# Kernel optimization log

Hardware: AMD Instinct MI355X
Metric: run time of the kernel (lower is better)

Reference implementation:

```python
import jax, jax.numpy as jnp
import numpy as np

D_MODEL = 512
D_STATE = 32
EXPAND = 2
D_INNER = D_MODEL * EXPAND
BATCH = 2
SEQ_LEN = 1024


def setup_inputs() -> dict:
    key = jax.random.key(0)
    ks = jax.random.split(key, 8)
    s = lambda fan_in: 1.0 / np.sqrt(fan_in)
    x = jax.random.normal(ks[0], (BATCH, SEQ_LEN, D_MODEL), dtype=jnp.float32)
    Wx = jax.random.uniform(ks[1], (D_INNER, D_MODEL), minval=-s(D_MODEL), maxval=s(D_MODEL))
    Wdt = jax.random.uniform(ks[2], (D_INNER, D_MODEL), minval=-s(D_MODEL), maxval=s(D_MODEL))
    bdt = jax.random.uniform(ks[3], (D_INNER,)) + 1.0  # dt_proj.bias init: rand + 1
    A_log = jnp.log(jax.random.uniform(ks[4], (D_INNER, D_STATE), minval=1e-4, maxval=1.0))
    WB = jax.random.uniform(ks[5], (D_INNER * D_STATE, D_MODEL), minval=-s(D_MODEL), maxval=s(D_MODEL))
    WC = jax.random.uniform(ks[6], (D_INNER * D_STATE, D_MODEL), minval=-s(D_MODEL), maxval=s(D_MODEL))
    Wout = jax.random.uniform(ks[7], (D_MODEL, D_INNER), minval=-s(D_INNER), maxval=s(D_INNER))
    return {"x": x, "Wx": Wx, "Wdt": Wdt, "bdt": bdt, "A_log": A_log,
            "WB": WB, "WC": WC, "Wout": Wout}


def reference(x, Wx, Wdt, bdt, A_log, WB, WC, Wout):
    b, L, _ = x.shape
    d_inner, d_state = A_log.shape

    x_inner = jnp.einsum('bld,ed->ble', x, Wx)                 # (b, L, d_inner)
    delta = jax.nn.softplus(jnp.einsum('bld,ed->ble', x, Wdt) + bdt)
    A = -jnp.exp(A_log.astype(jnp.float32))                    # (d_inner, d_state)
    A_disc = jnp.exp(delta[..., None] * A)                     # (b, L, d_inner, d_state)
    Bm = jnp.einsum('bld,ed->ble', x, WB).reshape(b, L, d_inner, d_state)
    Cm = jnp.einsum('bld,ed->ble', x, WC).reshape(b, L, d_inner, d_state)

    def step(h, inp):
        a_t, b_t, c_t, x_t = inp
        h = a_t * h + b_t * x_t[..., None]                     # (b, d_inner, d_state)
        y = jnp.sum(c_t * h, axis=-1)                          # (b, d_inner)
        return h, y

    h0 = jnp.zeros((b, d_inner, d_state), dtype=x.dtype)
    xs = (jnp.moveaxis(A_disc, 1, 0), jnp.moveaxis(Bm, 1, 0),
          jnp.moveaxis(Cm, 1, 0), jnp.moveaxis(x_inner, 1, 0))
    _, ys = jax.lax.scan(step, h0, xs)                         # ys: (L, b, d_inner)
    y = jnp.moveaxis(ys, 0, 1)
    y = y * jax.nn.sigmoid(y)                                  # SiLU
    return jnp.einsum('ble,de->bld', y, Wout)
```

## Files before the change

### kernel.cpp

```cpp
#include <hip/hip_runtime.h>

#define BATCH   2
#define SEQLEN  1024
#define DMODEL  512
#define DSTATE  32
#define DINNER  1024
#define MROWS   (BATCH*SEQLEN)
#define NPROJ   (2*DINNER + 2*DINNER*DSTATE)

typedef short bf16x8 __attribute__((ext_vector_type(8)));
typedef float f32x4  __attribute__((ext_vector_type(4)));

__device__ __forceinline__ unsigned short f2bf(float f) {
    union { float f; unsigned u; } c; c.f = f;
    unsigned u = c.u;
    u += 0x7fffu + ((u >> 16) & 1u);
    return (unsigned short)(u >> 16);
}
__device__ __forceinline__ float bf2f(unsigned short h) {
    union { unsigned u; float f; } c; c.u = ((unsigned)h) << 16;
    return c.f;
}

__global__ void cast_all(const float4* __restrict__ Wx, const float4* __restrict__ Wdt,
                         const float4* __restrict__ WB, const float4* __restrict__ WC,
                         const float4* __restrict__ x,  const float4* __restrict__ Wout,
                         unsigned short* __restrict__ Wbf,
                         unsigned short* __restrict__ Xbf,
                         unsigned short* __restrict__ Woutbf) {
    const long nWx = 131072, nWdt = 131072, nWB = 4194304, nWC = 4194304;
    const long nWall = nWx + nWdt + nWB + nWC;
    const long nX = 262144, nWo = 131072;
    const long total = nWall + nX + nWo;
    for (long u = (long)blockIdx.x * blockDim.x + threadIdx.x; u < total;
         u += (long)gridDim.x * blockDim.x) {
        float4 v; unsigned short* dst;
        if (u < nWall) {
            if (u < nWx)             v = Wx[u];
            else if (u < nWx+nWdt)   v = Wdt[u - nWx];
            else if (u < nWx+nWdt+nWB) v = WB[u - nWx - nWdt];
            else                     v = WC[u - nWx - nWdt - nWB];
            dst = Wbf + u*4;
        } else if (u < nWall + nX) {
            v = x[u - nWall];       dst = Xbf + (u - nWall)*4;
        } else {
            v = Wout[u - nWall - nX]; dst = Woutbf + (u - nWall - nX)*4;
        }
        ushort4 o; o.x = f2bf(v.x); o.y = f2bf(v.y); o.z = f2bf(v.z); o.w = f2bf(v.w);
        *(ushort4*)dst = o;
    }
}

template<int EPI>
__global__ __launch_bounds__(256)
void gemm_bt(const unsigned short* __restrict__ A, const unsigned short* __restrict__ Bw,
             int K, int N, int t0, int Tchunk,
             float* __restrict__ xin, float* __restrict__ dlt,
             unsigned short* __restrict__ Bout, unsigned short* __restrict__ Cout,
             const float* __restrict__ bdt, float* __restrict__ outf) {
    __shared__ unsigned short Asm[2][128*32];
    __shared__ unsigned short Bsm[2][128*32];
    const int tid  = threadIdx.x;
    const int w    = tid >> 6;
    const int lane = tid & 63;
    const int wm   = w >> 1, wn = w & 1;

    const int nx = gridDim.x, ny = gridDim.y;
    int ntile, rtile;
    if ((nx & 7) == 0) {
        const int lin = blockIdx.x + nx * blockIdx.y;
        const int xcd = lin & 7;
        const int sl  = lin >> 3;
        ntile = xcd * (nx >> 3) + sl / ny;
        rtile = sl % ny;
    } else {
        ntile = blockIdx.x; rtile = blockIdx.y;
    }

    const int rr0  = rtile * 128;
    const int bb   = (rr0 >= Tchunk) ? 1 : 0;
    const int grow0 = bb * SEQLEN + t0 + (rr0 - bb * Tchunk);
    const int n0   = ntile * 128;

    f32x4 acc[4][4] = {};

    const unsigned short* Ag = A  + (size_t)grow0 * K;
    const unsigned short* Bg = Bw + (size_t)n0 * K;

    const int c0 = w*64 + lane;
    const int c1 = c0 + 256;
    const int r   = lane & 15;
    const int h16 = lane >> 4;

    const int rowc0 = c0 >> 2, rowc1 = c1 >> 2;
    const int subc0 = (c0 & 3) ^ ((c0 >> 3) & 3);
    const int subc1 = (c1 & 3) ^ ((c1 >> 3) & 3);
    const size_t srcA0 = (size_t)rowc0 * K + subc0 * 8;
    const size_t srcA1 = (size_t)rowc1 * K + subc1 * 8;

    const int nt = K >> 5;

    #define STAGE(k0_, buf_)                                                              \
        do {                                                                              \
            __builtin_amdgcn_global_load_lds(                                             \
                (const __attribute__((address_space(1))) void*)(Ag + srcA0 + (k0_)),      \
                (__attribute__((address_space(3))) void*)(&Asm[(buf_)][w*512]), 16, 0, 0);\
            __builtin_amdgcn_global_load_lds(                                             \
                (const __attribute__((address_space(1))) void*)(Ag + srcA1 + (k0_)),      \
                (__attribute__((address_space(3))) void*)(&Asm[(buf_)][2048 + w*512]), 16, 0, 0); \
            __builtin_amdgcn_global_load_lds(                                             \
                (const __attribute__((address_space(1))) void*)(Bg + srcA0 + (k0_)),      \
                (__attribute__((address_space(3))) void*)(&Bsm[(buf_)][w*512]), 16, 0, 0);\
            __builtin_amdgcn_global_load_lds(                                             \
                (const __attribute__((address_space(1))) void*)(Bg + srcA1 + (k0_)),      \
                (__attribute__((address_space(3))) void*)(&Bsm[(buf_)][2048 + w*512]), 16, 0, 0); \
        } while (0)

    #define COMPUTE(buf_)                                                                 \
        do {                                                                              \
            bf16x8 af[4], bfr[4];                                                         \
            _Pragma("unroll")                                                             \
            for (int i = 0; i < 4; i++) {                                                 \
                const int Ra = wm*64 + i*16 + r;                                          \
                const int Rb = wn*64 + i*16 + r;                                          \
                af[i]  = *(const bf16x8*)(&Asm[(buf_)][Ra*32 + (h16 ^ ((Ra>>1)&3))*8]);   \
                bfr[i] = *(const bf16x8*)(&Bsm[(buf_)][Rb*32 + (h16 ^ ((Rb>>1)&3))*8]);   \
            }                                                                             \
            _Pragma("unroll")                                                             \
            for (int i = 0; i < 4; i++)                                                   \
                _Pragma("unroll")                                                         \
                for (int j = 0; j < 4; j++)                                               \
                    acc[i][j] = __builtin_amdgcn_mfma_f32_16x16x32_bf16(af[i], bfr[j], acc[i][j], 0, 0, 0); \
        } while (0)

    STAGE(0, 0);
    for (int it = 0; it < nt - 1; ++it) {
        const int cur = it & 1;
        STAGE((it + 1) * 32, cur ^ 1);
        asm volatile("s_waitcnt vmcnt(4)" ::: "memory");
        __builtin_amdgcn_s_barrier();
        COMPUTE(cur);
        asm volatile("" ::: "memory");
        __builtin_amdgcn_s_barrier();
        asm volatile("" ::: "memory");
    }
    asm volatile("s_waitcnt vmcnt(0)" ::: "memory");
    __builtin_amdgcn_s_barrier();
    COMPUTE((nt - 1) & 1);

    #undef STAGE
    #undef COMPUTE

    const int q = lane >> 4;
    #pragma unroll
    for (int i = 0; i < 4; i++) {
        const int lr0 = wm*64 + i*16 + q*4;
        #pragma unroll
        for (int j = 0; j < 4; j++) {
            const int ncol = n0 + wn*64 + j*16 + r;
            if (EPI == 0) {
                const int cr   = rr0 + lr0;
                const int lt   = cr - bb*Tchunk;
                const size_t tb = (size_t)(lt >> 3);
                const int tin  = lt & 7;
                if (ncol < 1024) {
                    float4 o = {acc[i][j][0], acc[i][j][1], acc[i][j][2], acc[i][j][3]};
                    *(float4*)(xin + ((size_t)bb*(SEQLEN/8) + (t0>>3) + tb)*8192 + ncol*8 + tin) = o;
                } else if (ncol < 2048) {
                    const float bias = bdt[ncol - 1024];
                    float4 o;
                    {   float z0 = acc[i][j][0] + bias; o.x = (z0 > 20.f) ? z0 : log1pf(__expf(z0));
                        float z1 = acc[i][j][1] + bias; o.y = (z1 > 20.f) ? z1 : log1pf(__expf(z1));
                        float z2 = acc[i][j][2] + bias; o.z = (z2 > 20.f) ? z2 : log1pf(__expf(z2));
                        float z3 = acc[i][j][3] + bias; o.w = (z3 > 20.f) ? z3 : log1pf(__expf(z3)); }
                    *(float4*)(dlt + ((size_t)bb*(SEQLEN/8) + (t0>>3) + tb)*8192 + (ncol-1024)*8 + tin) = o;
                } else if (ncol < 34816) {
                    const int cb = ncol - 2048;
                    short4 o;
                    o.x = (short)f2bf(acc[i][j][0]); o.y = (short)f2bf(acc[i][j][1]);
                    o.z = (short)f2bf(acc[i][j][2]); o.w = (short)f2bf(acc[i][j][3]);
                    *(short4*)(Bout + ((size_t)bb*(Tchunk>>3) + tb)*262144 + (size_t)cb*8 + tin) = o;
                } else {
                    const int cc = ncol - 34816;
                    short4 o;
                    o.x = (short)f2bf(acc[i][j][0]); o.y = (short)f2bf(acc[i][j][1]);
                    o.z = (short)f2bf(acc[i][j][2]); o.w = (short)f2bf(acc[i][j][3]);
                    *(short4*)(Cout + ((size_t)bb*(Tchunk>>3) + tb)*262144 + (size_t)cc*8 + tin) = o;
                }
            } else {
                #pragma unroll
                for (int t = 0; t < 4; t++)
                    outf[(size_t)(grow0 + lr0 + t)*N + ncol] = acc[i][j][t];
            }
        }
    }
}

__global__ __launch_bounds__(256)
void scan_seg1(const float* __restrict__ dlt, const float* __restrict__ xin,
               const unsigned short* __restrict__ Bbf,
               const float* __restrict__ A_log,
               float* __restrict__ sc_h, float* __restrict__ sc_a,
               int t0, int Tchunk, int SEG, int Tg) {
    const int tid = threadIdx.x;
    const int g = tid >> 5, s = tid & 31;
    const int G = blockIdx.x * 8 + g;
    const int seg = blockIdx.y;
    const int b = G >> 10, e = G & 1023;

    const float Aes = -__expf(A_log[e*32 + s]);
    float h = 0.f, ap = 1.f;

    const int NT  = Tg >> 3;
    const int gt0 = (t0 + seg*Tg) >> 3;
    const int ct0 = (seg*Tg) >> 3;
    const float* dxp = dlt + ((size_t)b*(SEQLEN/8) + gt0)*8192 + e*8;
    const float* xxp = xin + ((size_t)b*(SEQLEN/8) + gt0)*8192 + e*8;
    const unsigned short* bp = Bbf + ((size_t)b*(Tchunk>>3) + ct0)*262144 + (size_t)(e*32+s)*8;

    float4 d0 = *(const float4*)dxp, d1 = *(const float4*)(dxp+4);
    float4 x0 = *(const float4*)xxp, x1 = *(const float4*)(xxp+4);
    bf16x8 bv = *(const bf16x8*)bp;

    for (int k = 0; k < NT; ++k) {
        float4 nd0, nd1, nx0, nx1; bf16x8 nbv;
        if (k + 1 < NT) {
            const float* p1 = dxp + (size_t)(k+1)*8192;
            nd0 = *(const float4*)p1; nd1 = *(const float4*)(p1+4);
            const float* p2 = xxp + (size_t)(k+1)*8192;
            nx0 = *(const float4*)p2; nx1 = *(const float4*)(p2+4);
            nbv = *(const bf16x8*)(bp + (size_t)(k+1)*262144);
        }
        const float db[8] = {d0.x,d0.y,d0.z,d0.w,d1.x,d1.y,d1.z,d1.w};
        const float xb[8] = {x0.x,x0.y,x0.z,x0.w,x1.x,x1.y,x1.z,x1.w};
        #pragma unroll
        for (int j = 0; j < 8; j++) {
            const float a = __expf(db[j] * Aes);
            h = a*h + bf2f((unsigned short)bv[j])*xb[j];
            ap *= a;
        }
        if (k + 1 < NT) { d0=nd0; d1=nd1; x0=nx0; x1=nx1; bv=nbv; }
    }
    sc_h[((size_t)G*SEG + seg)*32 + s] = h;
    sc_a[((size_t)G*SEG + seg)*32 + s] = ap;
}

__global__ __launch_bounds__(256)
void scan_seg2(const float* __restrict__ sc_h, const float* __restrict__ sc_a,
               float* __restrict__ sc_hin, float* __restrict__ hbuf,
               int SEG, int first) {
    const int idx = blockIdx.x * 256 + threadIdx.x;
    float h = first ? 0.f : hbuf[idx];
    const int G = idx >> 5, s = idx & 31;
    for (int seg = 0; seg < SEG; seg++) {
        const size_t o = ((size_t)G*SEG + seg)*32 + s;
        sc_hin[o] = h;
        h = sc_h[o] + sc_a[o]*h;
    }
    hbuf[idx] = h;
}

__global__ __launch_bounds__(256)
void scan_seg3(const float* __restrict__ dlt, const float* __restrict__ xin,
               const unsigned short* __restrict__ Bbf, const unsigned short* __restrict__ Cbf,
               const float* __restrict__ A_log, const float* __restrict__ sc_hin,
               unsigned short* __restrict__ Ybf,
               int t0, int Tchunk, int SEG, int Tg) {
    const int tid = threadIdx.x;
    const int g = tid >> 5, s = tid & 31;
    const int G = blockIdx.x * 8 + g;
    const int seg = blockIdx.y;
    const int b = G >> 10, e = G & 1023;

    const float Aes = -__expf(A_log[e*32 + s]);
    float h = sc_hin[((size_t)G*SEG + seg)*32 + s];

    const int NT  = Tg >> 3;
    const int gt0 = (t0 + seg*Tg) >> 3;
    const int ct0 = (seg*Tg) >> 3;
    const float* dxp = dlt + ((size_t)b*(SEQLEN/8) + gt0)*8192 + e*8;
    const float* xxp = xin + ((size_t)b*(SEQLEN/8) + gt0)*8192 + e*8;
    const unsigned short* bp = Bbf + ((size_t)b*(Tchunk>>3) + ct0)*262144 + (size_t)(e*32+s)*8;
    const unsigned short* cp = Cbf + ((size_t)b*(Tchunk>>3) + ct0)*262144 + (size_t)(e*32+s)*8;
    const int tbase = t0 + seg*Tg;

    float4 d0 = *(const float4*)dxp, d1 = *(const float4*)(dxp+4);
    float4 x0 = *(const float4*)xxp, x1 = *(const float4*)(xxp+4);
    bf16x8 bv = *(const bf16x8*)bp, cv = *(const bf16x8*)cp;

    for (int k = 0; k < NT; ++k) {
        float4 nd0, nd1, nx0, nx1; bf16x8 nbv, ncv;
        if (k + 1 < NT) {
            const float* p1 = dxp + (size_t)(k+1)*8192;
            nd0 = *(const float4*)p1; nd1 = *(const float4*)(p1+4);
            const float* p2 = xxp + (size_t)(k+1)*8192;
            nx0 = *(const float4*)p2; nx1 = *(const float4*)(p2+4);
            nbv = *(const bf16x8*)(bp + (size_t)(k+1)*262144);
            ncv = *(const bf16x8*)(cp + (size_t)(k+1)*262144);
        }
        const float db[8] = {d0.x,d0.y,d0.z,d0.w,d1.x,d1.y,d1.z,d1.w};
        const float xb[8] = {x0.x,x0.y,x0.z,x0.w,x1.x,x1.y,x1.z,x1.w};
        float p[8];
        #pragma unroll
        for (int j = 0; j < 8; j++) {
            const float a = __expf(db[j] * Aes);
            h = a*h + bf2f((unsigned short)bv[j])*xb[j];
            p[j] = bf2f((unsigned short)cv[j])*h;
        }
        #pragma unroll
        for (int i = 0; i < 4; i++) {
            float send = (s & 16) ? p[i] : p[i+4];
            float recv = __shfl_xor(send, 16, 32);
            p[i] = ((s & 16) ? p[i+4] : p[i]) + recv;
        }
        #pragma unroll
        for (int i = 0; i < 2; i++) {
            float send = (s & 8) ? p[i] : p[i+2];
            float recv = __shfl_xor(send, 8, 32);
            p[i] = ((s & 8) ? p[i+2] : p[i]) + recv;
        }
        {
            float send = (s & 4) ? p[0] : p[1];
            float recv = __shfl_xor(send, 4, 32);
            p[0] = ((s & 4) ? p[1] : p[0]) + recv;
        }
        p[0] += __shfl_xor(p[0], 2, 32);
        p[0] += __shfl_xor(p[0], 1, 32);
        if ((s & 3) == 0) {
            const int tl = s >> 2;
            const float qv = p[0];
            const float y = qv * __builtin_amdgcn_rcpf(1.f + __expf(-qv));
            Ybf[(size_t)b*1048576 + e + (size_t)(tbase + k*8 + tl)*1024] = f2bf(y);
        }
        if (k + 1 < NT) { d0=nd0; d1=nd1; x0=nx0; x1=nx1; bv=nbv; cv=ncv; }
    }
}

extern "C" void kernel_launch(void* const* d_in, const int* in_sizes, int n_in,
                              void* d_out, int out_size, void* d_ws, size_t ws_size,
                              hipStream_t stream) {
    const float* x     = (const float*)d_in[0];
    const float* Wx    = (const float*)d_in[1];
    const float* Wdt   = (const float*)d_in[2];
    const float* bdt   = (const float*)d_in[3];
    const float* A_log = (const float*)d_in[4];
    const float* WB    = (const float*)d_in[5];
    const float* WC    = (const float*)d_in[6];
    const float* Wout  = (const float*)d_in[7];

    char* ws = (char*)d_ws;
    unsigned short* Wbf    = (unsigned short*)(ws);
    unsigned short* Xbf    = (unsigned short*)(ws + 69206016);
    unsigned short* Woutbf = (unsigned short*)(ws + 71303168);
    float*          xin    = (float*)        (ws + 72351744);
    float*          dlt    = (float*)        (ws + 80740352);
    unsigned short* Ybf    = (unsigned short*)(ws + 89128960);
    float*          hbuf   = (float*)        (ws + 93323264);
    float*          sc_h   = (float*)        (ws + 93585408);
    float*          sc_a   = (float*)        (ws + 95682560);
    float*          sc_hin = (float*)        (ws + 97779712);
    unsigned short* Bbf    = (unsigned short*)(ws + 99876864);
    const size_t fixedB = 99876864;

    int T = 128;
    const int cands[4] = {1024, 512, 256, 128};
    for (int ci = 0; ci < 4; ci++) {
        if (fixedB + (size_t)2 * cands[ci] * 131072 <= ws_size) { T = cands[ci]; break; }
    }
    unsigned short* Cbf = Bbf + (size_t)T * 65536;

    const int SEG = 8;
    const int Tg = T / SEG;

    cast_all<<<dim3(2048), dim3(256), 0, stream>>>(
        (const float4*)Wx, (const float4*)Wdt, (const float4*)WB, (const float4*)WC,
        (const float4*)x, (const float4*)Wout, Wbf, Xbf, Woutbf);

    const int NC = SEQLEN / T;
    for (int c = 0; c < NC; c++) {
        const int t0 = c * T;
        gemm_bt<0><<<dim3(NPROJ/128, 2*T/128), dim3(256), 0, stream>>>(
            Xbf, Wbf, DMODEL, NPROJ, t0, T, xin, dlt, Bbf, Cbf, bdt, nullptr);
        scan_seg1<<<dim3(256, SEG), dim3(256), 0, stream>>>(
            dlt, xin, Bbf, A_log, sc_h, sc_a, t0, T, SEG, Tg);
        scan_seg2<<<dim3(256), dim3(256), 0, stream>>>(
            sc_h, sc_a, sc_hin, hbuf, SEG, (c == 0) ? 1 : 0);
        scan_seg3<<<dim3(256, SEG), dim3(256), 0, stream>>>(
            dlt, xin, Bbf, Cbf, A_log, sc_hin, Ybf, t0, T, SEG, Tg);
    }

    gemm_bt<1><<<dim3(DMODEL/128, MROWS/128), dim3(256), 0, stream>>>(
        Ybf, Woutbf, DINNER, DMODEL, 0, MROWS, nullptr, nullptr, nullptr, nullptr, nullptr,
        (float*)d_out);
}
```

Measured before the change: 409.3 us.

## Store scan inputs segment-contiguous so each channel's time series is sequential

The projection GEMM epilogue now writes xin, delta, B and C in a layout grouped by (batch, segment, channel), with each channel's timesteps for one segment stored contiguously. Previously consecutive 8-step blocks sat 8192 or 262144 elements apart. Each scan thread now walks a short contiguous stream, which should improve cache and page locality for the scan kernels. In exchange the GEMM epilogue writes are more scattered, since different segments map to distant addresses. xin and delta are now chunk-local buffers.

```diff
diff --git a/kernel.cpp b/kernel.cpp
--- a/kernel.cpp
+++ b/kernel.cpp
@@ -54,7 +54,7 @@
 template<int EPI>
 __global__ __launch_bounds__(256)
 void gemm_bt(const unsigned short* __restrict__ A, const unsigned short* __restrict__ Bw,
-             int K, int N, int t0, int Tchunk,
+             int K, int N, int t0, int Tchunk, int tgs,
              float* __restrict__ xin, float* __restrict__ dlt,
              unsigned short* __restrict__ Bout, unsigned short* __restrict__ Cout,
              const float* __restrict__ bdt, float* __restrict__ outf) {
@@ -152,6 +152,8 @@
     #undef COMPUTE
 
     const int q = lane >> 4;
+    const int Tg  = 1 << tgs;
+    const int NT  = Tg >> 3;
     #pragma unroll
     for (int i = 0; i < 4; i++) {
         const int lr0 = wm*64 + i*16 + q*4;
@@ -161,11 +163,14 @@
             if (EPI == 0) {
                 const int cr   = rr0 + lr0;
                 const int lt   = cr - bb*Tchunk;
-                const size_t tb = (size_t)(lt >> 3);
-                const int tin  = lt & 7;
+                const int seg  = lt >> tgs;
+                const int tloc = lt & (Tg - 1);
+                const int kin  = tloc >> 3;
+                const int tin  = tloc & 7;
+                const int bs   = bb*8 + seg;
                 if (ncol < 1024) {
                     float4 o = {acc[i][j][0], acc[i][j][1], acc[i][j][2], acc[i][j][3]};
-                    *(float4*)(xin + ((size_t)bb*(SEQLEN/8) + (t0>>3) + tb)*8192 + ncol*8 + tin) = o;
+                    *(float4*)(xin + ((size_t)bs*1024 + ncol)*Tg + tloc) = o;
                 } else if (ncol < 2048) {
                     const float bias = bdt[ncol - 1024];
                     float4 o;
@@ -173,19 +178,19 @@
                         float z1 = acc[i][j][1] + bias; o.y = (z1 > 20.f) ? z1 : log1pf(__expf(z1));
                         float z2 = acc[i][j][2] + bias; o.z = (z2 > 20.f) ? z2 : log1pf(__expf(z2));
                         float z3 = acc[i][j][3] + bias; o.w = (z3 > 20.f) ? z3 : log1pf(__expf(z3)); }
-                    *(float4*)(dlt + ((size_t)bb*(SEQLEN/8) + (t0>>3) + tb)*8192 + (ncol-1024)*8 + tin) = o;
+                    *(float4*)(dlt + ((size_t)bs*1024 + (ncol-1024))*Tg + tloc) = o;
                 } else if (ncol < 34816) {
-                    const int cb = ncol - 2048;
+                    const int es = ncol - 2048;
                     short4 o;
                     o.x = (short)f2bf(acc[i][j][0]); o.y = (short)f2bf(acc[i][j][1]);
                     o.z = (short)f2bf(acc[i][j][2]); o.w = (short)f2bf(acc[i][j][3]);
-                    *(short4*)(Bout + ((size_t)bb*(Tchunk>>3) + tb)*262144 + (size_t)cb*8 + tin) = o;
+                    *(short4*)(Bout + (((size_t)bs*1024 + (es>>5))*NT + kin)*256 + (es&31)*8 + tin) = o;
                 } else {
-                    const int cc = ncol - 34816;
+                    const int es = ncol - 34816;
                     short4 o;
                     o.x = (short)f2bf(acc[i][j][0]); o.y = (short)f2bf(acc[i][j][1]);
                     o.z = (short)f2bf(acc[i][j][2]); o.w = (short)f2bf(acc[i][j][3]);
-                    *(short4*)(Cout + ((size_t)bb*(Tchunk>>3) + tb)*262144 + (size_t)cc*8 + tin) = o;
+                    *(short4*)(Cout + (((size_t)bs*1024 + (es>>5))*NT + kin)*256 + (es&31)*8 + tin) = o;
                 }
             } else {
                 #pragma unroll
@@ -201,7 +206,7 @@
                const unsigned short* __restrict__ Bbf,
                const float* __restrict__ A_log,
                float* __restrict__ sc_h, float* __restrict__ sc_a,
-               int t0, int Tchunk, int SEG, int Tg) {
+               int Tg) {
     const int tid = threadIdx.x;
     const int g = tid >> 5, s = tid & 31;
     const int G = blockIdx.x * 8 + g;
@@ -211,25 +216,22 @@
     const float Aes = -__expf(A_log[e*32 + s]);
     float h = 0.f, ap = 1.f;
 
-    const int NT  = Tg >> 3;
-    const int gt0 = (t0 + seg*Tg) >> 3;
-    const int ct0 = (seg*Tg) >> 3;
-    const float* dxp = dlt + ((size_t)b*(SEQLEN/8) + gt0)*8192 + e*8;
-    const float* xxp = xin + ((size_t)b*(SEQLEN/8) + gt0)*8192 + e*8;
-    const unsigned short* bp = Bbf + ((size_t)b*(Tchunk>>3) + ct0)*262144 + (size_t)(e*32+s)*8;
-
-    float4 d0 = *(const float4*)dxp, d1 = *(const float4*)(dxp+4);
-    float4 x0 = *(const float4*)xxp, x1 = *(const float4*)(xxp+4);
+    const int NT = Tg >> 3;
+    const int bs = b*8 + seg;
+    const float* dp = dlt + ((size_t)bs*1024 + e)*Tg;
+    const float* xp = xin + ((size_t)bs*1024 + e)*Tg;
+    const unsigned short* bp = Bbf + ((size_t)bs*1024 + e)*NT*256 + s*8;
+
+    float4 d0 = *(const float4*)dp, d1 = *(const float4*)(dp+4);
+    float4 x0 = *(const float4*)xp, x1 = *(const float4*)(xp+4);
     bf16x8 bv = *(const bf16x8*)bp;
 
     for (int k = 0; k < NT; ++k) {
         float4 nd0, nd1, nx0, nx1; bf16x8 nbv;
         if (k + 1 < NT) {
-            const float* p1 = dxp + (size_t)(k+1)*8192;
-            nd0 = *(const float4*)p1; nd1 = *(const float4*)(p1+4);
-            const float* p2 = xxp + (size_t)(k+1)*8192;
-            nx0 = *(const float4*)p2; nx1 = *(const float4*)(p2+4);
-            nbv = *(const bf16x8*)(bp + (size_t)(k+1)*262144);
+            nd0 = *(const float4*)(dp + (k+1)*8); nd1 = *(const float4*)(dp + (k+1)*8 + 4);
+            nx0 = *(const float4*)(xp + (k+1)*8); nx1 = *(const float4*)(xp + (k+1)*8 + 4);
+            nbv = *(const bf16x8*)(bp + (size_t)(k+1)*256);
         }
         const float db[8] = {d0.x,d0.y,d0.z,d0.w,d1.x,d1.y,d1.z,d1.w};
         const float xb[8] = {x0.x,x0.y,x0.z,x0.w,x1.x,x1.y,x1.z,x1.w};
@@ -241,19 +243,19 @@
         }
         if (k + 1 < NT) { d0=nd0; d1=nd1; x0=nx0; x1=nx1; bv=nbv; }
     }
-    sc_h[((size_t)G*SEG + seg)*32 + s] = h;
-    sc_a[((size_t)G*SEG + seg)*32 + s] = ap;
+    sc_h[((size_t)G*8 + seg)*32 + s] = h;
+    sc_a[((size_t)G*8 + seg)*32 + s] = ap;
 }
 
 __global__ __launch_bounds__(256)
 void scan_seg2(const float* __restrict__ sc_h, const float* __restrict__ sc_a,
                float* __restrict__ sc_hin, float* __restrict__ hbuf,
-               int SEG, int first) {
+               int first) {
     const int idx = blockIdx.x * 256 + threadIdx.x;
     float h = first ? 0.f : hbuf[idx];
     const int G = idx >> 5, s = idx & 31;
-    for (int seg = 0; seg < SEG; seg++) {
-        const size_t o = ((size_t)G*SEG + seg)*32 + s;
+    for (int seg = 0; seg < 8; seg++) {
+        const size_t o = ((size_t)G*8 + seg)*32 + s;
         sc_hin[o] = h;
         h = sc_h[o] + sc_a[o]*h;
     }
@@ -265,7 +267,7 @@
                const unsigned short* __restrict__ Bbf, const unsigned short* __restrict__ Cbf,
                const float* __restrict__ A_log, const float* __restrict__ sc_hin,
                unsigned short* __restrict__ Ybf,
-               int t0, int Tchunk, int SEG, int Tg) {
+               int t0, int Tg) {
     const int tid = threadIdx.x;
     const int g = tid >> 5, s = tid & 31;
     const int G = blockIdx.x * 8 + g;
@@ -273,30 +275,27 @@
     const int b = G >> 10, e = G & 1023;
 
     const float Aes = -__expf(A_log[e*32 + s]);
-    float h = sc_hin[((size_t)G*SEG + seg)*32 + s];
-
-    const int NT  = Tg >> 3;
-    const int gt0 = (t0 + seg*Tg) >> 3;
-    const int ct0 = (seg*Tg) >> 3;
-    const float* dxp = dlt + ((size_t)b*(SEQLEN/8) + gt0)*8192 + e*8;
-    const float* xxp = xin + ((size_t)b*(SEQLEN/8) + gt0)*8192 + e*8;
-    const unsigned short* bp = Bbf + ((size_t)b*(Tchunk>>3) + ct0)*262144 + (size_t)(e*32+s)*8;
-    const unsigned short* cp = Cbf + ((size_t)b*(Tchunk>>3) + ct0)*262144 + (size_t)(e*32+s)*8;
+    float h = sc_hin[((size_t)G*8 + seg)*32 + s];
+
+    const int NT = Tg >> 3;
+    const int bs = b*8 + seg;
+    const float* dp = dlt + ((size_t)bs*1024 + e)*Tg;
+    const float* xp = xin + ((size_t)bs*1024 + e)*Tg;
+    const unsigned short* bp = Bbf + ((size_t)bs*1024 + e)*NT*256 + s*8;
+    const unsigned short* cp = Cbf + ((size_t)bs*1024 + e)*NT*256 + s*8;
     const int tbase = t0 + seg*Tg;
 
-    float4 d0 = *(const float4*)dxp, d1 = *(const float4*)(dxp+4);
-    float4 x0 = *(const float4*)xxp, x1 = *(const float4*)(xxp+4);
+    float4 d0 = *(const float4*)dp, d1 = *(const float4*)(dp+4);
+    float4 x0 = *(const float4*)xp, x1 = *(const float4*)(xp+4);
     bf16x8 bv = *(const bf16x8*)bp, cv = *(const bf16x8*)cp;
 
     for (int k = 0; k < NT; ++k) {
         float4 nd0, nd1, nx0, nx1; bf16x8 nbv, ncv;
         if (k + 1 < NT) {
-            const float* p1 = dxp + (size_t)(k+1)*8192;
-            nd0 = *(const float4*)p1; nd1 = *(const float4*)(p1+4);
-            const float* p2 = xxp + (size_t)(k+1)*8192;
-            nx0 = *(const float4*)p2; nx1 = *(const float4*)(p2+4);
-            nbv = *(const bf16x8*)(bp + (size_t)(k+1)*262144);
-            ncv = *(const bf16x8*)(cp + (size_t)(k+1)*262144);
+            nd0 = *(const float4*)(dp + (k+1)*8); nd1 = *(const float4*)(dp + (k+1)*8 + 4);
+            nx0 = *(const float4*)(xp + (k+1)*8); nx1 = *(const float4*)(xp + (k+1)*8 + 4);
+            nbv = *(const bf16x8*)(bp + (size_t)(k+1)*256);
+            ncv = *(const bf16x8*)(cp + (size_t)(k+1)*256);
         }
         const float db[8] = {d0.x,d0.y,d0.z,d0.w,d1.x,d1.y,d1.z,d1.w};
         const float xb[8] = {x0.x,x0.y,x0.z,x0.w,x1.x,x1.y,x1.z,x1.w};
@@ -369,8 +368,8 @@
     }
     unsigned short* Cbf = Bbf + (size_t)T * 65536;
 
-    const int SEG = 8;
-    const int Tg = T / SEG;
+    const int Tg = T / 8;
+    int tgs = 0; while ((1 << tgs) < Tg) tgs++;
 
     cast_all<<<dim3(2048), dim3(256), 0, stream>>>(
         (const float4*)Wx, (const float4*)Wdt, (const float4*)WB, (const float4*)WC,
@@ -380,16 +379,16 @@
     for (int c = 0; c < NC; c++) {
         const int t0 = c * T;
         gemm_bt<0><<<dim3(NPROJ/128, 2*T/128), dim3(256), 0, stream>>>(
-            Xbf, Wbf, DMODEL, NPROJ, t0, T, xin, dlt, Bbf, Cbf, bdt, nullptr);
-        scan_seg1<<<dim3(256, SEG), dim3(256), 0, stream>>>(
-            dlt, xin, Bbf, A_log, sc_h, sc_a, t0, T, SEG, Tg);
+            Xbf, Wbf, DMODEL, NPROJ, t0, T, tgs, xin, dlt, Bbf, Cbf, bdt, nullptr);
+        scan_seg1<<<dim3(256, 8), dim3(256), 0, stream>>>(
+            dlt, xin, Bbf, A_log, sc_h, sc_a, Tg);
         scan_seg2<<<dim3(256), dim3(256), 0, stream>>>(
-            sc_h, sc_a, sc_hin, hbuf, SEG, (c == 0) ? 1 : 0);
-        scan_seg3<<<dim3(256, SEG), dim3(256), 0, stream>>>(
-            dlt, xin, Bbf, Cbf, A_log, sc_hin, Ybf, t0, T, SEG, Tg);
+            sc_h, sc_a, sc_hin, hbuf, (c == 0) ? 1 : 0);
+        scan_seg3<<<dim3(256, 8), dim3(256), 0, stream>>>(
+            dlt, xin, Bbf, Cbf, A_log, sc_hin, Ybf, t0, Tg);
     }
 
     gemm_bt<1><<<dim3(DMODEL/128, MROWS/128), dim3(256), 0, stream>>>(
-        Ybf, Woutbf, DINNER, DMODEL, 0, MROWS, nullptr, nullptr, nullptr, nullptr, nullptr,
+        Ybf, Woutbf, DINNER, DMODEL, 0, MROWS, 0, nullptr, nullptr, nullptr, nullptr, nullptr,
         (float*)d_out);
 }
```

New measurement: 413.8 us. No clear change (+1.1%).
